# Kernel tuning notes

Measured on AMD Instinct MI355X. Metric: run time of the kernel, lower is better.

The kernel has to match this reference:

```python
import jax, jax.numpy as jnp
import numpy as np
from jax import lax

D_TEMPORAL, D_INNER, D_STATE, D_CONV, DT_RANK = 2, 4, 16, 4, 1
EPS = 1e-5


def setup_inputs() -> dict:
    key = jax.random.key(0)
    ks = jax.random.split(key, 14)
    B, L = 16, 32768
    f = lambda k, s, scale=1.0: jax.random.normal(k, s, jnp.float32) * scale
    dt_b = float(np.log(np.expm1(0.01)))  # softplus^-1(0.01), typical dt init
    A_log = jnp.log(jnp.tile(jnp.arange(1, D_STATE + 1, dtype=jnp.float32), (D_INNER, 1)))
    return {
        "hidden_states": f(ks[0], (B, D_TEMPORAL, L)),
        "norm_w": jnp.ones((D_TEMPORAL,), jnp.float32),
        "in_proj_w": f(ks[1], (2 * D_INNER, D_TEMPORAL), 0.5),
        "conv_w": f(ks[2], (D_INNER, D_CONV), 0.3),
        "conv_b": f(ks[3], (D_INNER,), 0.1),
        "x_proj_w": f(ks[4], (DT_RANK + 2 * D_STATE, D_INNER), 0.3),
        "dt_proj_w": f(ks[5], (D_INNER, DT_RANK), 1.0),
        "dt_proj_b": jnp.full((D_INNER,), dt_b, jnp.float32),
        "A_log": A_log,
        "D": jnp.ones((D_INNER,), jnp.float32),
        "conv_w_b": f(ks[6], (D_INNER, D_CONV), 0.3),
        "conv_b_b": f(ks[7], (D_INNER,), 0.1),
        "x_proj_w_b": f(ks[8], (DT_RANK + 2 * D_STATE, D_INNER), 0.3),
        "dt_proj_w_b": f(ks[9], (D_INNER, DT_RANK), 1.0),
        "dt_proj_b_b": jnp.full((D_INNER,), dt_b, jnp.float32),
        "A_b_log": A_log,
        "D_b": jnp.ones((D_INNER,), jnp.float32),
        "out_proj_w": f(ks[10], (D_TEMPORAL, D_INNER), 0.3),
        "norm_f_w": jnp.ones((D_TEMPORAL,), jnp.float32),
    }


def _silu(x):
    return x * jax.nn.sigmoid(x)


def _rmsnorm(x, w):
    return x * lax.rsqrt(jnp.mean(x * x, axis=-1, keepdims=True) + EPS) * w


def _branch(x, z, conv_w, conv_b, x_proj_w, dt_proj_w, dt_proj_b, A_log, D):
    # x, z: (B, d_inner, L). Causal depthwise conv + silu.
    Bb, d, L = x.shape
    xc = lax.conv_general_dilated(
        x, conv_w[:, None, :], (1,), [(D_CONV - 1, 0)],
        feature_group_count=d, dimension_numbers=("NCH", "OIH", "NCH"))
    u = _silu(xc + conv_b[None, :, None]).transpose(0, 2, 1)      # (B, L, d)
    x_dbl = u @ x_proj_w.T                                        # (B, L, rank+2n)
    dt, Bm, Cm = jnp.split(x_dbl, [DT_RANK, DT_RANK + D_STATE], axis=-1)
    dt = jax.nn.softplus(dt @ dt_proj_w.T + dt_proj_b)            # (B, L, d)
    A = -jnp.exp(A_log)                                           # (d, n)
    dA = jnp.exp(dt[..., None] * A)                               # (B, L, d, n)
    dBu = (dt * u)[..., None] * Bm[:, :, None, :]                 # (B, L, d, n)

    def step(h, inp):
        dA_t, dBu_t, C_t = inp
        h = dA_t * h + dBu_t                                      # (B, d, n)
        return h, jnp.einsum("bdn,bn->bd", h, C_t)

    h0 = jnp.zeros((Bb, d, D_STATE), dtype=u.dtype)
    _, ys = lax.scan(step, h0, (jnp.swapaxes(dA, 0, 1), jnp.swapaxes(dBu, 0, 1), jnp.swapaxes(Cm, 0, 1)))
    y = jnp.swapaxes(ys, 0, 1) + u * D                            # (B, L, d)
    return y * _silu(z.transpose(0, 2, 1))


def _forward(hidden_states, norm_w, in_proj_w, conv_w, conv_b, x_proj_w, dt_proj_w,
             dt_proj_b, A_log, D, conv_w_b, conv_b_b, x_proj_w_b, dt_proj_w_b,
             dt_proj_b_b, A_b_log, D_b, out_proj_w, norm_f_w):
    # hidden_states: (B, T=d_temporal, L); scan runs over L.
    hs = jnp.swapaxes(hidden_states, 1, 2)                        # (B, L, T)
    residual = hs.astype(jnp.float32)
    hs = _rmsnorm(residual, norm_w)
    xz = jnp.swapaxes(hs @ in_proj_w.T, 1, 2)                     # (B, 2*d_inner, L)
    x, z = jnp.split(xz, 2, axis=1)
    y_f = _branch(x, z, conv_w, conv_b, x_proj_w, dt_proj_w, dt_proj_b, A_log, D)
    y_b = _branch(x[..., ::-1], z[..., ::-1], conv_w_b, conv_b_b, x_proj_w_b,
                  dt_proj_w_b, dt_proj_b_b, A_b_log, D_b)
    y = y_f + y_b[:, ::-1, :]                                     # (B, L, d_inner)
    out = y @ out_proj_w.T                                        # (B, L, T)
    out = _rmsnorm(out + residual, norm_f_w)
    return jnp.swapaxes(out, 1, 2)                                # (B, T, L)


def reference(hidden_states, norm_w, in_proj_w, conv_w, conv_b, x_proj_w, dt_proj_w,
              dt_proj_b, A_log, D, conv_w_b, conv_b_b, x_proj_w_b, dt_proj_w_b,
              dt_proj_b_b, A_b_log, D_b, out_proj_w, norm_f_w):
    return _forward(hidden_states, norm_w, in_proj_w, conv_w, conv_b, x_proj_w,
                    dt_proj_w, dt_proj_b, A_log, D, conv_w_b, conv_b_b, x_proj_w_b,
                    dt_proj_w_b, dt_proj_b_b, A_b_log, D_b, out_proj_w, norm_f_w)
```

## Files before the change

kernel.cpp:

```cpp
#include <hip/hip_runtime.h>
#include <cstdint>

#define BB 16
#define LL 32768
#define NC 512

#define WD_SZ 256
#define XPW 0
#define CVW 132
#define CVB 148
#define DTW 152
#define DTB 156
#define AW  160
#define DW  224
#define G_INPROJ 512
#define G_NORMW 528
#define G_OUTP 530
#define G_NORMF 538
#define FLG 1000

#define PQ_OFF 4096
#define PQ_BYTES ((size_t)BB*2*NC*64*8)
#define HIN_OFF (PQ_OFF + PQ_BYTES)

#define LOG2E 1.4426950408889634f

__device__ __forceinline__ float bf2f(unsigned short u){ return __uint_as_float(((unsigned int)u)<<16); }
__device__ __forceinline__ float blo(unsigned int u){ return __uint_as_float(u<<16); }
__device__ __forceinline__ float bhi(unsigned int u){ return __uint_as_float(u & 0xffff0000u); }
__device__ __forceinline__ unsigned short f2bf(float f){
  unsigned int x = __float_as_uint(f);
  x += 0x7fffu + ((x>>16)&1u);
  return (unsigned short)(x>>16);
}
__device__ __forceinline__ unsigned int pack2(float a, float b){
  return (unsigned int)f2bf(a) | ((unsigned int)f2bf(b)<<16);
}
__device__ __forceinline__ float siluf(float x){ return x / (1.f + __expf(-x)); }
__device__ __forceinline__ float softplusf_(float x){ return fmaxf(x,0.f) + log1pf(__expf(-fabsf(x))); }

__device__ __forceinline__ float exp2fast(float x){
#if __has_builtin(__builtin_amdgcn_exp2f)
  return __builtin_amdgcn_exp2f(x);
#else
  float r; asm("v_exp_f32 %0, %1\ns_nop 0" : "=v"(r) : "v"(x)); return r;
#endif
}

__device__ __forceinline__ float rowsum16(float x){
  union { float f; int i; } a, t;
  a.f = x;
  t.i = __builtin_amdgcn_update_dpp(0, a.i, 0x121, 0xf, 0xf, true); a.f += t.f;
  t.i = __builtin_amdgcn_update_dpp(0, a.i, 0x122, 0xf, 0xf, true); a.f += t.f;
  t.i = __builtin_amdgcn_update_dpp(0, a.i, 0x124, 0xf, 0xf, true); a.f += t.f;
  t.i = __builtin_amdgcn_update_dpp(0, a.i, 0x128, 0xf, 0xf, true); a.f += t.f;
  return a.f;
}

__device__ __forceinline__ float ldw(const void* p, int i, int isf){
  return isf ? ((const float*)p)[i] : bf2f(((const unsigned short*)p)[i]);
}
__device__ __forceinline__ float2 hid2(const void* hid, int isf, int b, int t){
  if (isf){
    const float* p = (const float*)hid;
    return make_float2(p[(size_t)b*2*LL + t], p[(size_t)b*2*LL + LL + t]);
  }
  const unsigned short* p = (const unsigned short*)hid;
  return make_float2(bf2f(p[(size_t)b*2*LL + t]), bf2f(p[(size_t)b*2*LL + LL + t]));
}
__device__ __forceinline__ float4 xrow(const void* __restrict__ hid, int isf,
                                       const float* __restrict__ W, int b, int t){
  float2 h = hid2(hid, isf, b, t);
  float ms = rsqrtf(0.5f*(h.x*h.x + h.y*h.y) + 1e-5f);
  float v0 = h.x*ms*W[G_NORMW], v1 = h.y*ms*W[G_NORMW+1];
  float4 x;
  x.x = W[G_INPROJ+0]*v0 + W[G_INPROJ+1]*v1;
  x.y = W[G_INPROJ+2]*v0 + W[G_INPROJ+3]*v1;
  x.z = W[G_INPROJ+4]*v0 + W[G_INPROJ+5]*v1;
  x.w = W[G_INPROJ+6]*v0 + W[G_INPROJ+7]*v1;
  return x;
}

__global__ void k_prep(const void* __restrict__ normw, const void* __restrict__ inpj,
    const void* __restrict__ cwf, const void* __restrict__ cbf,
    const void* __restrict__ xpf, const void* __restrict__ dwf,
    const void* __restrict__ dbf, const void* __restrict__ alf,
    const void* __restrict__ ddf,
    const void* __restrict__ cwb, const void* __restrict__ cbb,
    const void* __restrict__ xpb, const void* __restrict__ dwb,
    const void* __restrict__ dbb, const void* __restrict__ alb,
    const void* __restrict__ ddb,
    const void* __restrict__ outp, const void* __restrict__ nfw,
    float* __restrict__ W)
{
  const int isf = (((const unsigned int*)ddf)[0] == 0x3F800000u) ? 1 : 0;
  int t = threadIdx.x;
  for (int i=t;i<132;i+=256){ W[XPW+i]=ldw(xpf,i,isf); W[WD_SZ+XPW+i]=ldw(xpb,i,isf); }
  for (int i=t;i<16;i+=256){ W[CVW+i]=ldw(cwf,i,isf); W[WD_SZ+CVW+i]=ldw(cwb,i,isf); W[G_INPROJ+i]=ldw(inpj,i,isf); }
  for (int i=t;i<4;i+=256){
    W[CVB+i]=ldw(cbf,i,isf); W[WD_SZ+CVB+i]=ldw(cbb,i,isf);
    W[DTW+i]=ldw(dwf,i,isf); W[WD_SZ+DTW+i]=ldw(dwb,i,isf);
    W[DTB+i]=ldw(dbf,i,isf); W[WD_SZ+DTB+i]=ldw(dbb,i,isf);
    W[DW+i] =ldw(ddf,i,isf); W[WD_SZ+DW+i] =ldw(ddb,i,isf);
  }
  for (int i=t;i<64;i+=256){
    W[AW+i]       = -__expf(ldw(alf,i,isf)) * LOG2E;
    W[WD_SZ+AW+i] = -__expf(ldw(alb,i,isf)) * LOG2E;
  }
  for (int i=t;i<8;i+=256) W[G_OUTP+i]=ldw(outp,i,isf);
  for (int i=t;i<2;i+=256){ W[G_NORMW+i]=ldw(normw,i,isf); W[G_NORMF+i]=ldw(nfw,i,isf); }
  if (t==0) W[FLG] = (float)isf;
}

template<int DR>
__device__ __forceinline__ float2 scan_chunk(const float (* __restrict__ dtPd)[68],
    const unsigned short (* __restrict__ dtud)[68],
    const unsigned short (* __restrict__ bpd)[68],
    float Ax, int d, int n)
{
  float P=1.f, Q=0.f;
  for (int j4=0; j4<16; j4++){
    const int t0 = DR ? 60-4*j4 : 4*j4;
    float4  d4 = *(const float4*)&dtPd[d][t0];
    ushort4 u4 = *(const ushort4*)&dtud[d][t0];
    ushort4 b4 = *(const ushort4*)&bpd[n][t0];
    float da[4]={d4.x,d4.y,d4.z,d4.w};
    unsigned short ua[4]={u4.x,u4.y,u4.z,u4.w};
    unsigned short ba[4]={b4.x,b4.y,b4.z,b4.w};
    #pragma unroll
    for (int jr=0; jr<4; jr++){
      const int k = DR ? 3-jr : jr;
      float e = exp2fast(Ax*da[k]);
      P *= e;
      Q = fmaf(Q, e, bf2f(ua[k])*bf2f(ba[k]));
    }
  }
  return make_float2(P,Q);
}

template<int DR>
__device__ __forceinline__ void scan_fused(const float (* __restrict__ dtPd)[68],
    const unsigned short (* __restrict__ dtud)[68],
    const unsigned int (* __restrict__ bcd)[68],
    float (* __restrict__ ySd)[68],
    float h, float Ax, int d, int n)
{
  for (int j4=0; j4<16; j4++){
    const int t0 = DR ? 60-4*j4 : 4*j4;
    float4  d4 = *(const float4*)&dtPd[d][t0];
    ushort4 u4 = *(const ushort4*)&dtud[d][t0];
    uint4   c4 = *(const uint4*)&bcd[n][t0];
    float da[4]={d4.x,d4.y,d4.z,d4.w};
    unsigned short ua[4]={u4.x,u4.y,u4.z,u4.w};
    unsigned int ca[4]={c4.x,c4.y,c4.z,c4.w};
    float s[4];
    #pragma unroll
    for (int jr=0; jr<4; jr++){
      const int k = DR ? 3-jr : jr;
      float e = exp2fast(Ax*da[k]);
      h = fmaf(e, h, bf2f(ua[k])*blo(ca[k]));
      s[k] = rowsum16(h*bhi(ca[k]));
    }
    if (n == 0) *(float4*)&ySd[d][t0] = make_float4(s[0],s[1],s[2],s[3]);
  }
}

__global__ __launch_bounds__(128, 4) void k_chunk(const void* __restrict__ hid,
    const float* __restrict__ W, float2* __restrict__ PQ)
{
  __shared__ __align__(16) float4 xb[70];
  __shared__ __align__(16) float dtP[2][4][68];
  __shared__ __align__(16) unsigned short dtuP[2][4][68];
  __shared__ __align__(16) unsigned short Bp[2][16][68];
  const int tid  = threadIdx.x;
  const int wid  = tid >> 6;
  const int lane = tid & 63;
  const int gid  = blockIdx.x;
  const int c    = gid & (NC-1);
  const int b    = gid >> 9;
  const int isf  = (int)W[FLG];

  if (wid == 0){
    int t = c*64 + lane;
    xb[lane+3] = xrow(hid, isf, W, b, t);
    if (lane < 3){
      int t2 = c*64 - 3 + lane;
      float4 v = make_float4(0.f,0.f,0.f,0.f);
      if (t2 >= 0) v = xrow(hid, isf, W, b, t2);
      xb[lane] = v;
    }
    if (lane >= 61){
      int t3 = c*64 + lane + 3;
      float4 v = make_float4(0.f,0.f,0.f,0.f);
      if (t3 < LL) v = xrow(hid, isf, W, b, t3);
      xb[lane+6] = v;
    }
  }
  __syncthreads();
  {
    const float* Wd = W + wid*WD_SZ;
    float4 a0,a1,a2,a3;
    if (wid == 0){ a0=xb[lane];   a1=xb[lane+1]; a2=xb[lane+2]; a3=xb[lane+3]; }
    else         { a0=xb[lane+6]; a1=xb[lane+5]; a2=xb[lane+4]; a3=xb[lane+3]; }
    float u[4];
    u[0] = siluf(Wd[CVB+0] + Wd[CVW+ 0]*a0.x + Wd[CVW+ 1]*a1.x + Wd[CVW+ 2]*a2.x + Wd[CVW+ 3]*a3.x);
    u[1] = siluf(Wd[CVB+1] + Wd[CVW+ 4]*a0.y + Wd[CVW+ 5]*a1.y + Wd[CVW+ 6]*a2.y + Wd[CVW+ 7]*a3.y);
    u[2] = siluf(Wd[CVB+2] + Wd[CVW+ 8]*a0.z + Wd[CVW+ 9]*a1.z + Wd[CVW+10]*a2.z + Wd[CVW+11]*a3.z);
    u[3] = siluf(Wd[CVB+3] + Wd[CVW+12]*a0.w + Wd[CVW+13]*a1.w + Wd[CVW+14]*a2.w + Wd[CVW+15]*a3.w);
    float dtr = Wd[XPW+0]*u[0] + Wd[XPW+1]*u[1] + Wd[XPW+2]*u[2] + Wd[XPW+3]*u[3];
    #pragma unroll
    for (int d2=0; d2<4; d2++){
      float dt = softplusf_(fmaf(Wd[DTW+d2], dtr, Wd[DTB+d2]));
      dtP[wid][d2][lane]  = dt;
      dtuP[wid][d2][lane] = f2bf(dt*u[d2]);
    }
    #pragma unroll
    for (int n=0; n<16; n++){
      float Bn = Wd[XPW+(1+n)*4+0]*u[0] + Wd[XPW+(1+n)*4+1]*u[1]
               + Wd[XPW+(1+n)*4+2]*u[2] + Wd[XPW+(1+n)*4+3]*u[3];
      Bp[wid][n][lane] = f2bf(Bn);
    }
  }
  __syncthreads();
  const int d = lane>>4, n = lane&15;
  const float Ax = W[wid*WD_SZ + AW + d*16 + n];
  float2 pq;
  size_t idx;
  if (wid == 0){
    pq  = scan_chunk<0>(dtP[0], dtuP[0], Bp[0], Ax, d, n);
    idx = ((size_t)(b*2+0)*NC + c);
  } else {
    pq  = scan_chunk<1>(dtP[1], dtuP[1], Bp[1], Ax, d, n);
    idx = ((size_t)(b*2+1)*NC + (NC-1-c));
  }
  PQ[idx*64 + lane] = pq;
}

__global__ __launch_bounds__(64) void k_scan(const float2* __restrict__ PQ, float* __restrict__ hin)
{
  int bd = blockIdx.x; int lane = threadIdx.x;
  float h = 0.f;
  size_t base = (size_t)bd*NC;
  for (int c0=0; c0<NC; c0+=16){
    float2 v[16];
    #pragma unroll
    for (int k=0;k<16;k++) v[k] = PQ[(base+c0+k)*64 + lane];
    #pragma unroll
    for (int k=0;k<16;k++){
      hin[(base+c0+k)*64 + lane] = h;
      h = fmaf(v[k].x, h, v[k].y);
    }
  }
}

__global__ __launch_bounds__(128, 4) void k_fused(const void* __restrict__ hid,
    const float* __restrict__ W, const float* __restrict__ hin,
    void* __restrict__ out)
{
  __shared__ __align__(16) char smx[2176];
  __shared__ __align__(16) float dtP[2][4][68];
  __shared__ __align__(16) unsigned short dtuP[2][4][68];
  __shared__ __align__(16) unsigned int BCp[2][16][68];
  __shared__ __align__(16) float zs[256];
  __shared__ __align__(16) float uD2[2][256];
  float4* xb = (float4*)smx;
  float (*yS)[4][68] = (float (*)[4][68])smx;

  const int tid  = threadIdx.x;
  const int wid  = tid >> 6;
  const int lane = tid & 63;
  const int gid  = blockIdx.x;
  const int c    = gid & (NC-1);
  const int b    = gid >> 9;
  const int isf  = (int)W[FLG];

  const int rc = wid ? (NC-1-c) : c;
  float h0 = hin[((size_t)(b*2+wid)*NC + rc)*64 + lane];

  if (wid == 0){
    int t = c*64 + lane;
    xb[lane+3] = xrow(hid, isf, W, b, t);
    if (lane < 3){
      int t2 = c*64 - 3 + lane;
      float4 v = make_float4(0.f,0.f,0.f,0.f);
      if (t2 >= 0) v = xrow(hid, isf, W, b, t2);
      xb[lane] = v;
    }
    if (lane >= 61){
      int t3 = c*64 + lane + 3;
      float4 v = make_float4(0.f,0.f,0.f,0.f);
      if (t3 < LL) v = xrow(hid, isf, W, b, t3);
      xb[lane+6] = v;
    }
  } else {
    int t = c*64 + lane;
    float2 hh = hid2(hid, isf, b, t);
    float ms = rsqrtf(0.5f*(hh.x*hh.x + hh.y*hh.y) + 1e-5f);
    float v0 = hh.x*ms*W[G_NORMW], v1 = hh.y*ms*W[G_NORMW+1];
    float4 z4;
    z4.x = siluf(W[G_INPROJ+ 8]*v0 + W[G_INPROJ+ 9]*v1);
    z4.y = siluf(W[G_INPROJ+10]*v0 + W[G_INPROJ+11]*v1);
    z4.z = siluf(W[G_INPROJ+12]*v0 + W[G_INPROJ+13]*v1);
    z4.w = siluf(W[G_INPROJ+14]*v0 + W[G_INPROJ+15]*v1);
    *(float4*)&zs[lane*4] = z4;
  }
  __syncthreads();
  {
    const float* Wd = W + wid*WD_SZ;
    float4 a0,a1,a2,a3;
    if (wid == 0){ a0=xb[lane];   a1=xb[lane+1]; a2=xb[lane+2]; a3=xb[lane+3]; }
    else         { a0=xb[lane+6]; a1=xb[lane+5]; a2=xb[lane+4]; a3=xb[lane+3]; }
    float u[4];
    u[0] = siluf(Wd[CVB+0] + Wd[CVW+ 0]*a0.x + Wd[CVW+ 1]*a1.x + Wd[CVW+ 2]*a2.x + Wd[CVW+ 3]*a3.x);
    u[1] = siluf(Wd[CVB+1] + Wd[CVW+ 4]*a0.y + Wd[CVW+ 5]*a1.y + Wd[CVW+ 6]*a2.y + Wd[CVW+ 7]*a3.y);
    u[2] = siluf(Wd[CVB+2] + Wd[CVW+ 8]*a0.z + Wd[CVW+ 9]*a1.z + Wd[CVW+10]*a2.z + Wd[CVW+11]*a3.z);
    u[3] = siluf(Wd[CVB+3] + Wd[CVW+12]*a0.w + Wd[CVW+13]*a1.w + Wd[CVW+14]*a2.w + Wd[CVW+15]*a3.w);
    float dtr = Wd[XPW+0]*u[0] + Wd[XPW+1]*u[1] + Wd[XPW+2]*u[2] + Wd[XPW+3]*u[3];
    float4 ud4;
    #pragma unroll
    for (int d2=0; d2<4; d2++){
      float dt = softplusf_(fmaf(Wd[DTW+d2], dtr, Wd[DTB+d2]));
      dtP[wid][d2][lane]  = dt;
      dtuP[wid][d2][lane] = f2bf(dt*u[d2]);
      ((float*)&ud4)[d2] = u[d2]*Wd[DW+d2];
    }
    *(float4*)&uD2[wid][lane*4] = ud4;
    #pragma unroll
    for (int n=0; n<16; n++){
      float Bn = Wd[XPW+(1+n)*4+0]*u[0] + Wd[XPW+(1+n)*4+1]*u[1]
               + Wd[XPW+(1+n)*4+2]*u[2] + Wd[XPW+(1+n)*4+3]*u[3];
      float Cn = Wd[XPW+(17+n)*4+0]*u[0] + Wd[XPW+(17+n)*4+1]*u[1]
               + Wd[XPW+(17+n)*4+2]*u[2] + Wd[XPW+(17+n)*4+3]*u[3];
      BCp[wid][n][lane] = pack2(Bn, Cn);
    }
  }
  __syncthreads();

  const int d = lane>>4, n = lane&15;
  const float Ax = W[wid*WD_SZ + AW + d*16 + n];
  if (wid == 0) scan_fused<0>(dtP[0], dtuP[0], BCp[0], yS[0], h0, Ax, d, n);
  else          scan_fused<1>(dtP[1], dtuP[1], BCp[1], yS[1], h0, Ax, d, n);
  __syncthreads();

  {
    int t = c*64 + lane;
    float4 zz = *(const float4*)&zs[lane*4];
    float4 u0 = *(const float4*)&uD2[0][lane*4];
    float4 u1 = *(const float4*)&uD2[1][lane*4];
    float y0 = (yS[0][0][lane] + yS[1][0][lane] + u0.x + u1.x) * zz.x;
    float y1 = (yS[0][1][lane] + yS[1][1][lane] + u0.y + u1.y) * zz.y;
    float y2 = (yS[0][2][lane] + yS[1][2][lane] + u0.z + u1.z) * zz.z;
    float y3 = (yS[0][3][lane] + yS[1][3][lane] + u0.w + u1.w) * zz.w;
    float o0 = W[G_OUTP+0]*y0 + W[G_OUTP+1]*y1 + W[G_OUTP+2]*y2 + W[G_OUTP+3]*y3;
    float o1 = W[G_OUTP+4]*y0 + W[G_OUTP+5]*y1 + W[G_OUTP+6]*y2 + W[G_OUTP+7]*y3;
    float2 r = hid2(hid, isf, b, t);
    o0 += r.x;
    o1 += r.y;
    float ms = rsqrtf(0.5f*(o0*o0 + o1*o1) + 1e-5f);
    float e0 = o0*ms*W[G_NORMF], e1 = o1*ms*W[G_NORMF+1];
    size_t i0 = (size_t)b*2*LL + t, i1 = i0 + LL;
    if (isf){
      if (wid == 0) ((float*)out)[i0] = e0;
      else          ((float*)out)[i1] = e1;
    } else {
      if (wid == 0) ((unsigned short*)out)[i0] = f2bf(e0);
      else          ((unsigned short*)out)[i1] = f2bf(e1);
    }
  }
}

extern "C" void kernel_launch(void* const* d_in, const int* in_sizes, int n_in,
                              void* d_out, int out_size, void* d_ws, size_t ws_size,
                              hipStream_t stream)
{
  (void)in_sizes; (void)n_in; (void)out_size; (void)ws_size;
  const void* hid   = d_in[0];
  const void* normw = d_in[1];
  const void* inpj  = d_in[2];
  const void* cwf   = d_in[3];
  const void* cbf   = d_in[4];
  const void* xpf   = d_in[5];
  const void* dwf   = d_in[6];
  const void* dbf   = d_in[7];
  const void* alf   = d_in[8];
  const void* ddf   = d_in[9];
  const void* cwb   = d_in[10];
  const void* cbb   = d_in[11];
  const void* xpb   = d_in[12];
  const void* dwb   = d_in[13];
  const void* dbb   = d_in[14];
  const void* alb   = d_in[15];
  const void* ddb   = d_in[16];
  const void* outp  = d_in[17];
  const void* nfw   = d_in[18];

  float* W   = (float*)d_ws;
  float2* PQ = (float2*)((char*)d_ws + PQ_OFF);
  float* hin = (float*)((char*)d_ws + HIN_OFF);

  k_prep<<<1,256,0,stream>>>(normw, inpj, cwf, cbf, xpf, dwf, dbf, alf, ddf,
                             cwb, cbb, xpb, dwb, dbb, alb, ddb, outp, nfw, W);
  k_chunk<<<BB*NC, 128, 0, stream>>>(hid, W, PQ);
  k_scan<<<BB*2, 64, 0, stream>>>(PQ, hin);
  k_fused<<<BB*NC, 128, 0, stream>>>(hid, W, hin, d_out);
}
```

Measured before the change: 196.0 us.

## Parallelize inter-chunk scan across waves and use hardware bf16 pack conversions

The inter-chunk state scan now runs with 8 waves per (batch,direction) block instead of one. Each wave first reduces its slice of chunks to an affine (A,B) pair, then applies the prefix of earlier waves' pairs before rescanning its slice. This removes a long serial latency chain on 32 tiny blocks at the cost of reading PQ twice. Float-to-bf16 rounding now uses the v_cvt_pk_bf16_f32 instruction, and the row sum uses inline DPP adds with explicit nops, which trims ALU work in the chunk and fused kernels.

```diff
diff --git a/kernel.cpp b/kernel.cpp
--- a/kernel.cpp
+++ b/kernel.cpp
@@ -28,14 +28,16 @@
 __device__ __forceinline__ float bf2f(unsigned short u){ return __uint_as_float(((unsigned int)u)<<16); }
 __device__ __forceinline__ float blo(unsigned int u){ return __uint_as_float(u<<16); }
 __device__ __forceinline__ float bhi(unsigned int u){ return __uint_as_float(u & 0xffff0000u); }
-__device__ __forceinline__ unsigned short f2bf(float f){
-  unsigned int x = __float_as_uint(f);
-  x += 0x7fffu + ((x>>16)&1u);
-  return (unsigned short)(x>>16);
-}
-__device__ __forceinline__ unsigned int pack2(float a, float b){
-  return (unsigned int)f2bf(a) | ((unsigned int)f2bf(b)<<16);
-}
+
+__device__ __forceinline__ unsigned int cvtpk(float lo, float hi){
+  unsigned int r;
+  asm("v_cvt_pk_bf16_f32 %0, %1, %2" : "=v"(r) : "v"(lo), "v"(hi));
+  return r;
+}
+__device__ __forceinline__ unsigned short cvt1(float x){
+  return (unsigned short)cvtpk(x, x);
+}
+
 __device__ __forceinline__ float siluf(float x){ return x / (1.f + __expf(-x)); }
 __device__ __forceinline__ float softplusf_(float x){ return fmaxf(x,0.f) + log1pf(__expf(-fabsf(x))); }
 
@@ -48,13 +50,16 @@
 }
 
 __device__ __forceinline__ float rowsum16(float x){
-  union { float f; int i; } a, t;
-  a.f = x;
-  t.i = __builtin_amdgcn_update_dpp(0, a.i, 0x121, 0xf, 0xf, true); a.f += t.f;
-  t.i = __builtin_amdgcn_update_dpp(0, a.i, 0x122, 0xf, 0xf, true); a.f += t.f;
-  t.i = __builtin_amdgcn_update_dpp(0, a.i, 0x124, 0xf, 0xf, true); a.f += t.f;
-  t.i = __builtin_amdgcn_update_dpp(0, a.i, 0x128, 0xf, 0xf, true); a.f += t.f;
-  return a.f;
+  asm("s_nop 1\n\t"
+      "v_add_f32_dpp %0, %0, %0 row_ror:1 row_mask:0xf bank_mask:0xf\n\t"
+      "s_nop 1\n\t"
+      "v_add_f32_dpp %0, %0, %0 row_ror:2 row_mask:0xf bank_mask:0xf\n\t"
+      "s_nop 1\n\t"
+      "v_add_f32_dpp %0, %0, %0 row_ror:4 row_mask:0xf bank_mask:0xf\n\t"
+      "s_nop 1\n\t"
+      "v_add_f32_dpp %0, %0, %0 row_ror:8 row_mask:0xf bank_mask:0xf"
+      : "+v"(x));
+  return x;
 }
 
 __device__ __forceinline__ float ldw(const void* p, int i, int isf){
@@ -212,13 +217,13 @@
     for (int d2=0; d2<4; d2++){
       float dt = softplusf_(fmaf(Wd[DTW+d2], dtr, Wd[DTB+d2]));
       dtP[wid][d2][lane]  = dt;
-      dtuP[wid][d2][lane] = f2bf(dt*u[d2]);
+      dtuP[wid][d2][lane] = cvt1(dt*u[d2]);
     }
     #pragma unroll
     for (int n=0; n<16; n++){
       float Bn = Wd[XPW+(1+n)*4+0]*u[0] + Wd[XPW+(1+n)*4+1]*u[1]
                + Wd[XPW+(1+n)*4+2]*u[2] + Wd[XPW+(1+n)*4+3]*u[3];
-      Bp[wid][n][lane] = f2bf(Bn);
+      Bp[wid][n][lane] = cvt1(Bn);
     }
   }
   __syncthreads();
@@ -236,12 +241,29 @@
   PQ[idx*64 + lane] = pq;
 }
 
-__global__ __launch_bounds__(64) void k_scan(const float2* __restrict__ PQ, float* __restrict__ hin)
-{
-  int bd = blockIdx.x; int lane = threadIdx.x;
+#define SCAN_WAVES 8
+#define SCAN_CPW (NC/SCAN_WAVES)
+__global__ __launch_bounds__(512) void k_scan(const float2* __restrict__ PQ, float* __restrict__ hin)
+{
+  __shared__ float As[SCAN_WAVES][64];
+  __shared__ float Bs[SCAN_WAVES][64];
+  const int bd = blockIdx.x;
+  const int lane = threadIdx.x & 63;
+  const int w    = threadIdx.x >> 6;
+  const size_t base = (size_t)bd*NC + (size_t)w*SCAN_CPW;
+  float A = 1.f, Bc = 0.f;
+  for (int c0=0; c0<SCAN_CPW; c0+=16){
+    float2 v[16];
+    #pragma unroll
+    for (int k=0;k<16;k++) v[k] = PQ[(base+c0+k)*64 + lane];
+    #pragma unroll
+    for (int k=0;k<16;k++){ A *= v[k].x; Bc = fmaf(v[k].x, Bc, v[k].y); }
+  }
+  As[w][lane] = A; Bs[w][lane] = Bc;
+  __syncthreads();
   float h = 0.f;
-  size_t base = (size_t)bd*NC;
-  for (int c0=0; c0<NC; c0+=16){
+  for (int j=0;j<w;j++) h = fmaf(As[j][lane], h, Bs[j][lane]);
+  for (int c0=0; c0<SCAN_CPW; c0+=16){
     float2 v[16];
     #pragma unroll
     for (int k=0;k<16;k++) v[k] = PQ[(base+c0+k)*64 + lane];
@@ -321,7 +343,7 @@
     for (int d2=0; d2<4; d2++){
       float dt = softplusf_(fmaf(Wd[DTW+d2], dtr, Wd[DTB+d2]));
       dtP[wid][d2][lane]  = dt;
-      dtuP[wid][d2][lane] = f2bf(dt*u[d2]);
+      dtuP[wid][d2][lane] = cvt1(dt*u[d2]);
       ((float*)&ud4)[d2] = u[d2]*Wd[DW+d2];
     }
     *(float4*)&uD2[wid][lane*4] = ud4;
@@ -331,7 +353,7 @@
                + Wd[XPW+(1+n)*4+2]*u[2] + Wd[XPW+(1+n)*4+3]*u[3];
       float Cn = Wd[XPW+(17+n)*4+0]*u[0] + Wd[XPW+(17+n)*4+1]*u[1]
                + Wd[XPW+(17+n)*4+2]*u[2] + Wd[XPW+(17+n)*4+3]*u[3];
-      BCp[wid][n][lane] = pack2(Bn, Cn);
+      BCp[wid][n][lane] = cvtpk(Bn, Cn);
     }
   }
   __syncthreads();
@@ -363,8 +385,8 @@
       if (wid == 0) ((float*)out)[i0] = e0;
       else          ((float*)out)[i1] = e1;
     } else {
-      if (wid == 0) ((unsigned short*)out)[i0] = f2bf(e0);
-      else          ((unsigned short*)out)[i1] = f2bf(e1);
+      if (wid == 0) ((unsigned short*)out)[i0] = cvt1(e0);
+      else          ((unsigned short*)out)[i1] = cvt1(e1);
     }
   }
 }
@@ -401,6 +423,6 @@
   k_prep<<<1,256,0,stream>>>(normw, inpj, cwf, cbf, xpf, dwf, dbf, alf, ddf,
                              cwb, cbb, xpb, dwb, dbb, alb, ddb, outp, nfw, W);
   k_chunk<<<BB*NC, 128, 0, stream>>>(hid, W, PQ);
-  k_scan<<<BB*2, 64, 0, stream>>>(PQ, hin);
+  k_scan<<<BB*2, 512, 0, stream>>>(PQ, hin);
   k_fused<<<BB*NC, 128, 0, stream>>>(hid, W, hin, d_out);
 }
```

New measurement: 194.0 us. About the same (-1.0%).
